# Kernel optimization log

Measured on AMD Instinct MI355X. Metric: run time of the kernel, lower is better.

The kernel has to match this reference:

```python
import jax, jax.numpy as jnp
import numpy as np

N_USERS = 100000
N_ITEMS = 50000
N_LAYERS = 3
LATENT_DIM = 64
N_INTERACTIONS = 600000
BATCH = 4096
N_TOTAL = N_USERS + N_ITEMS


def setup_inputs() -> dict:
    key = jax.random.key(0)
    k_e, k_u, k_p, k_n = jax.random.split(key, 4)

    # --- build bipartite interaction graph (numpy, host-side like scipy in the original) ---
    rng = np.random.default_rng(0)
    u = rng.integers(0, N_USERS, size=N_INTERACTIONS)
    i = rng.integers(0, N_ITEMS, size=N_INTERACTIONS) + N_USERS
    # symmetrize: A[u, i] = 1 and A[i, u] = 1
    row = np.concatenate([u, i]).astype(np.int32)
    col = np.concatenate([i, u]).astype(np.int32)
    # symmetric degree normalization: D^{-1/2} A D^{-1/2}
    deg = np.bincount(row, minlength=N_TOTAL).astype(np.float32)
    d_inv = np.power(deg + 1e-9, -0.5)
    d_inv[np.isinf(d_inv)] = 0.0
    vals = (d_inv[row] * d_inv[col]).astype(np.float32)

    # Xavier-uniform init for E0 (fan_in = fan_out = dims of the weight matrix)
    limit = float(np.sqrt(6.0 / (N_TOTAL + LATENT_DIM)))
    E0 = jax.random.uniform(k_e, (N_TOTAL, LATENT_DIM), jnp.float32, -limit, limit)

    return {
        "users": jax.random.randint(k_u, (BATCH,), 0, N_USERS),
        "pos_items": jax.random.randint(k_p, (BATCH,), 0, N_ITEMS),
        "neg_items": jax.random.randint(k_n, (BATCH,), 0, N_ITEMS),
        "E0": E0,
        "adj_row": jnp.asarray(row),
        "adj_col": jnp.asarray(col),
        "adj_vals": jnp.asarray(vals),
    }


def reference(users, pos_items, neg_items, E0, adj_row, adj_col, adj_vals):
    # SpMM via gather + segment-sum: out[r] = sum_{e: row[e]=r} vals[e] * E[col[e]]
    def spmm(E):
        return jax.ops.segment_sum(adj_vals[:, None] * E[adj_col], adj_row,
                                   num_segments=N_TOTAL)

    # layer propagation with running sum (mean over layer stack)
    E_k = E0
    acc = E0
    for _ in range(N_LAYERS):
        E_k = spmm(E_k)
        acc = acc + E_k
    final_emb = acc / (N_LAYERS + 1)  # [N_TOTAL, D]

    user_emb = final_emb[:N_USERS]
    item_emb = final_emb[N_USERS:]

    u_emb = user_emb[users]
    pos_emb = item_emb[pos_items]
    neg_emb = item_emb[neg_items]
    u_emb0 = E0[users]
    pos_emb0 = E0[N_USERS + pos_items]
    neg_emb0 = E0[N_USERS + neg_items]
    return (u_emb, pos_emb, neg_emb, u_emb0, pos_emb0, neg_emb0)
```

## Files before the change

kernel.cpp:

```cpp
#include <hip/hip_runtime.h>
#include <hip/hip_fp16.h>

#define LATENT 64
#define N_USERS_C 100000

#define BROWS 128
#define LOG_BROWS 7
#define NBUCK_MAX 1280
#define NBLKA_MAX 512
#define SORT_T 256
#define SORT_E 16
#define SORT_CHUNK (SORT_T * SORT_E)
#define BUCK_CAP 4608

typedef unsigned short ushort8_t __attribute__((ext_vector_type(8)));

__device__ __forceinline__ unsigned enc_val14(float v) {
    unsigned vb = (unsigned)__float_as_int(v) + 0x1000u;
    return (((vb >> 23) - 0x77u) << 10) | ((vb >> 13) & 0x3FFu);
}
__device__ __forceinline__ float dec_val14(unsigned m) {
    return __uint_as_float(m ? ((((m >> 10) + 0x77u) << 23) | ((m & 0x3FFu) << 13)) : 0u);
}


__global__ void sortA_conv_kernel(const int* __restrict__ row, const int* __restrict__ col,
                                  const float* __restrict__ vals,
                                  unsigned* __restrict__ aux, unsigned char* __restrict__ rowloc,
                                  int* __restrict__ cntmat, int* __restrict__ srcmat,
                                  int* __restrict__ bcnt, int nnz, int nbuck, int nblkA,
                                  const float* __restrict__ E0, __half* __restrict__ E0h,
                                  int n4) {
    __shared__ int cnt[NBUCK_MAX];
    __shared__ int off[NBUCK_MAX];
    __shared__ int part[SORT_T];
    __shared__ unsigned buf[SORT_CHUNK];
    __shared__ unsigned char rbuf[SORT_CHUNK];
    int t = threadIdx.x;

    if (blockIdx.x >= nblkA) {
        int cb = blockIdx.x - nblkA;
        int base4 = cb * (SORT_T * 4);
#pragma unroll
        for (int jj = 0; jj < 4; jj++) {
            int i = base4 + jj * SORT_T + t;
            if (i < n4) {
                float4 v = ((const float4*)E0)[i];
                __half2* o = (__half2*)E0h;
                o[2 * i]     = __floats2half2_rn(v.x, v.y);
                o[2 * i + 1] = __floats2half2_rn(v.z, v.w);
            }
        }
        return;
    }

    int blk = blockIdx.x;
    int base = blk * SORT_CHUNK;

    for (int i = t; i < nbuck; i += SORT_T) cnt[i] = 0;
    __syncthreads();

    int      eb[SORT_E];
    unsigned pl[SORT_E];
    unsigned char rl8[SORT_E];
#pragma unroll
    for (int j = 0; j < SORT_E; j++) {
        int e = base + j * SORT_T + t;
        if (e < nnz) {
            int r = row[e];
            int b = r >> LOG_BROWS;
            eb[j] = b;
            pl[j] = (unsigned)col[e] | (enc_val14(vals[e]) << 18);
            rl8[j] = (unsigned char)(r & (BROWS - 1));
            atomicAdd(&cnt[b], 1);
        } else {
            eb[j] = -1;
        }
    }
    __syncthreads();

    int chunk = (nbuck + SORT_T - 1) / SORT_T;
    int lo = t * chunk, hi = lo + chunk; if (hi > nbuck) hi = nbuck;
    int s = 0;
    for (int i = lo; i < hi; i++) s += cnt[i];
    part[t] = s;
    __syncthreads();
    for (int o = 1; o < SORT_T; o <<= 1) {
        int x = (t >= o) ? part[t - o] : 0;
        __syncthreads();
        part[t] += x;
        __syncthreads();
    }
    int run = (t == 0) ? 0 : part[t - 1];
    for (int i = lo; i < hi; i++) { off[i] = run; run += cnt[i]; }
    __syncthreads();

#pragma unroll
    for (int j = 0; j < SORT_E; j++) {
        if (eb[j] >= 0) {
            int p = atomicAdd(&off[eb[j]], 1);
            buf[p] = pl[j];
            rbuf[p] = rl8[j];
        }
    }
    __syncthreads();

    for (int b = t; b < nbuck; b += SORT_T) {
        int c = cnt[b];
        int beg = off[b] - c;
        cntmat[(size_t)blk * nbuck + b] = c;
        srcmat[(size_t)blk * nbuck + b] = beg;
        if (c) atomicAdd(&bcnt[b], c);
    }
    int nvalid = nnz - base; if (nvalid > SORT_CHUNK) nvalid = SORT_CHUNK;
    for (int i = t; i < nvalid; i += SORT_T) {
        aux[base + i] = buf[i];
        rowloc[base + i] = rbuf[i];
    }
}


__global__ void sortB_kernel(const unsigned* __restrict__ aux,
                             const unsigned char* __restrict__ rowloc,
                             const int* __restrict__ cntmat, const int* __restrict__ srcmat,
                             const int* __restrict__ bcnt,
                             unsigned* __restrict__ edges, int* __restrict__ startOut,
                             int* __restrict__ origRow, int* __restrict__ slotOfRow,
                             int nblkA, int nbuck, int ntotal, int nnz) {
    __shared__ int rs[NBLKA_MAX], roff[NBLKA_MAX + 1];
    __shared__ int part[SORT_T];
    __shared__ unsigned buf[BUCK_CAP];
    __shared__ unsigned char rbuf[BUCK_CAP];
    __shared__ int cnt128[BROWS];
    __shared__ int slotOf[BROWS];
    __shared__ int rowOf[BROWS];
    __shared__ int offS[BROWS];
    __shared__ int placeOff[BROWS];
    __shared__ int dhist[64];
    int b = blockIdx.x, t = threadIdx.x;

    int sb = 0;
    for (int i = t; i < b; i += SORT_T) sb += bcnt[i];
    part[t] = sb;
    __syncthreads();
    for (int o = 1; o < SORT_T; o <<= 1) {
        int x = (t >= o) ? part[t - o] : 0;
        __syncthreads();
        part[t] += x;
        __syncthreads();
    }
    int base = part[SORT_T - 1];
    int tot = bcnt[b];
    __syncthreads();

    int rbase = b * BROWS;
    int nr = ntotal - rbase; if (nr > BROWS) nr = BROWS;

    int chunk = (nblkA + SORT_T - 1) / SORT_T;
    int lo = t * chunk, hi = lo + chunk; if (hi > nblkA) hi = nblkA;
    int rcl[8];
    int s = 0;
    for (int i = lo; i < hi; i++) {
        int c = cntmat[(size_t)i * nbuck + b];
        rcl[i - lo] = c;
        rs[i] = srcmat[(size_t)i * nbuck + b];
        s += c;
    }
    part[t] = s;
    if (t < BROWS) cnt128[t] = 0;
    if (t < 64) dhist[t] = 0;
    __syncthreads();
    for (int o = 1; o < SORT_T; o <<= 1) {
        int x = (t >= o) ? part[t - o] : 0;
        __syncthreads();
        part[t] += x;
        __syncthreads();
    }
    int run = (t == 0) ? 0 : part[t - 1];
    for (int i = lo; i < hi; i++) { roff[i] = run; run += rcl[i - lo]; }
    if (t == SORT_T - 1) roff[nblkA] = part[SORT_T - 1];
    __syncthreads();

    for (int i = t; i < tot; i += SORT_T) {
        int lo2 = 0, hi2 = nblkA;
        while (hi2 - lo2 > 1) {
            int mid = (lo2 + hi2) >> 1;
            if (roff[mid] <= i) lo2 = mid; else hi2 = mid;
        }
        size_t src = (size_t)lo2 * SORT_CHUNK + rs[lo2] + (i - roff[lo2]);
        buf[i] = aux[src];
        unsigned char rl = rowloc[src];
        rbuf[i] = rl;
        atomicAdd(&cnt128[rl], 1);
    }
    __syncthreads();

    if (t < nr) { int d = min(cnt128[t], 63); atomicAdd(&dhist[d], 1); }
    __syncthreads();
    part[t] = (t < 64) ? dhist[t] : 0;
    __syncthreads();
    for (int o = 1; o < 64; o <<= 1) {
        int x = (t >= o) ? part[t - o] : 0;
        __syncthreads();
        part[t] += x;
        __syncthreads();
    }
    if (t < 64) dhist[t] = (t == 0) ? 0 : part[t - 1];
    __syncthreads();
    if (t < nr) {
        int d = min(cnt128[t], 63);
        int sl = atomicAdd(&dhist[d], 1);
        slotOf[t] = sl;
        rowOf[sl] = t;
    }
    __syncthreads();

    part[t] = (t < nr) ? cnt128[rowOf[t]] : 0;
    __syncthreads();
    for (int o = 1; o < SORT_T; o <<= 1) {
        int x = (t >= o) ? part[t - o] : 0;
        __syncthreads();
        part[t] += x;
        __syncthreads();
    }
    if (t < nr) offS[t] = (t == 0) ? 0 : part[t - 1];
    __syncthreads();

    if (t < nr) {
        startOut[rbase + t]   = base + offS[t];
        origRow[rbase + t]    = rbase + rowOf[t];
        slotOfRow[rbase + t]  = rbase + slotOf[t];
        placeOff[t] = offS[slotOf[t]];
    }
    if (b == nbuck - 1 && t == 0) startOut[ntotal] = nnz;
    __syncthreads();

    for (int i = t; i < tot; i += SORT_T) {
        int p = atomicAdd(&placeOff[rbuf[i]], 1);
        edges[base + p] = buf[i];
    }
}


__global__ void spmm_slot(const int* __restrict__ start, const int* __restrict__ origRow,
                          const unsigned* __restrict__ edges,
                          const __half* __restrict__ Ein, __half* __restrict__ Eout,
                          int nslots) {
    int t = blockIdx.x * blockDim.x + threadIdx.x;
    int w = t >> 6;
    int lane = t & 63;
    int g = lane >> 3, l = lane & 7;
    int s = 8 * w + g;
    if (s >= nslots) return;
    int b = start[s];
    int e = start[s + 1];
    int ro = origRow[s];
    float a0 = 0.f, a1 = 0.f, a2 = 0.f, a3 = 0.f;
    float a4 = 0.f, a5 = 0.f, a6 = 0.f, a7 = 0.f;
    for (int k = (b & ~3); k < e; k += 4) {
        uint4 ev = *(const uint4*)(edges + k);
        unsigned ed[4] = { ev.x, ev.y, ev.z, ev.w };
#pragma unroll
        for (int j = 0; j < 4; j++) {
            int kk = k + j;
            if (kk < b || kk >= e) ed[j] = 0u;
        }
        ushort8_t gv[4];
#pragma unroll
        for (int j = 0; j < 4; j++) {
            gv[j] = *(const ushort8_t*)(Ein + (size_t)(ed[j] & 0x3FFFFu) * LATENT + 8 * l);
        }
#pragma unroll
        for (int j = 0; j < 4; j++) {
            float wv = dec_val14(ed[j] >> 18);
            const __half2* h2 = (const __half2*)&gv[j];
            a0 += wv * __low2float(h2[0]);
            a1 += wv * __high2float(h2[0]);
            a2 += wv * __low2float(h2[1]);
            a3 += wv * __high2float(h2[1]);
            a4 += wv * __low2float(h2[2]);
            a5 += wv * __high2float(h2[2]);
            a6 += wv * __low2float(h2[3]);
            a7 += wv * __high2float(h2[3]);
        }
    }
    union { ushort8_t u; __half2 h[4]; } o;
    o.h[0] = __floats2half2_rn(a0, a1);
    o.h[1] = __floats2half2_rn(a2, a3);
    o.h[2] = __floats2half2_rn(a4, a5);
    o.h[3] = __floats2half2_rn(a6, a7);
    *(ushort8_t*)(Eout + (size_t)ro * LATENT + 8 * l) = o.u;
}


__global__ void fin_fused(const int* __restrict__ users, const int* __restrict__ pos,
                          const int* __restrict__ neg,
                          const int* __restrict__ start, const int* __restrict__ slotOfRow,
                          const unsigned* __restrict__ edges,
                          const float* __restrict__ E0, const __half* __restrict__ E1,
                          const __half* __restrict__ E2,
                          float* __restrict__ out, int batch) {
    int t = blockIdx.x * blockDim.x + threadIdx.x;
    int w = t >> 6;
    int lane = t & 63;
    int g = lane >> 4, l = lane & 15;
    int i = 4 * w + g;
    int nent = 3 * batch;
    if (i >= nent) return;
    int grp = i / batch;
    int bb = i - grp * batch;
    int r = (grp == 0) ? users[bb] : (grp == 1) ? (N_USERS_C + pos[bb]) : (N_USERS_C + neg[bb]);
    int s = slotOfRow[r];
    int b = start[s];
    int e = start[s + 1];
    float a0 = 0.f, a1 = 0.f, a2 = 0.f, a3 = 0.f;
    for (int k = (b & ~3); k < e; k += 4) {
        uint4 ev = *(const uint4*)(edges + k);
        unsigned ed[4] = { ev.x, ev.y, ev.z, ev.w };
#pragma unroll
        for (int j = 0; j < 4; j++) {
            int kk = k + j;
            if (kk < b || kk >= e) ed[j] = 0u;
        }
        ushort4 gv[4];
#pragma unroll
        for (int j = 0; j < 4; j++) {
            gv[j] = *(const ushort4*)(E2 + (size_t)(ed[j] & 0x3FFFFu) * LATENT + 4 * l);
        }
#pragma unroll
        for (int j = 0; j < 4; j++) {
            float wv = dec_val14(ed[j] >> 18);
            const __half2* h2 = (const __half2*)&gv[j];
            a0 += wv * __low2float(h2[0]);
            a1 += wv * __high2float(h2[0]);
            a2 += wv * __low2float(h2[1]);
            a3 += wv * __high2float(h2[1]);
        }
    }
    size_t idx = (size_t)r * LATENT + 4 * l;
    float4 e0v = *(const float4*)(E0 + idx);
    ushort4 e1u = *(const ushort4*)(E1 + idx);
    ushort4 e2u = *(const ushort4*)(E2 + idx);
    const __half2* h1 = (const __half2*)&e1u;
    const __half2* h2v = (const __half2*)&e2u;
    float4 res;
    res.x = 0.25f * (e0v.x + __low2float(h1[0])  + __low2float(h2v[0])  + a0);
    res.y = 0.25f * (e0v.y + __high2float(h1[0]) + __high2float(h2v[0]) + a1);
    res.z = 0.25f * (e0v.z + __low2float(h1[1])  + __low2float(h2v[1])  + a2);
    res.w = 0.25f * (e0v.w + __high2float(h1[1]) + __high2float(h2v[1]) + a3);
    int total = nent * LATENT;
    *(float4*)(out + (size_t)i * LATENT + 4 * l) = res;
    *(float4*)(out + total + (size_t)i * LATENT + 4 * l) = e0v;
}

extern "C" void kernel_launch(void* const* d_in, const int* in_sizes, int n_in,
                              void* d_out, int out_size, void* d_ws, size_t ws_size,
                              hipStream_t stream) {
    const int*   users = (const int*)d_in[0];
    const int*   pos   = (const int*)d_in[1];
    const int*   neg   = (const int*)d_in[2];
    const float* E0    = (const float*)d_in[3];
    const int*   row   = (const int*)d_in[4];
    const int*   col   = (const int*)d_in[5];
    const float* vals  = (const float*)d_in[6];
    float*       out   = (float*)d_out;

    const int batch  = in_sizes[0];
    const int nnz    = in_sizes[4];
    const int ntotal = in_sizes[3] / LATENT;
    const int nbuck  = (ntotal + BROWS - 1) / BROWS;
    const int nblkA  = (nnz + SORT_CHUNK - 1) / SORT_CHUNK;

    auto align256 = [](size_t x) { return (x + 255) & ~(size_t)255; };

    const size_t hbufBytes = align256((size_t)ntotal * LATENT * sizeof(__half));
    const size_t edgeBytes = align256((size_t)nnz * sizeof(unsigned) + 16);
    const size_t auxBytes  = align256((size_t)nnz * sizeof(unsigned));
    const size_t matBytes  = align256((size_t)nblkA * nbuck * sizeof(int));
    const size_t stBytes   = align256((size_t)(ntotal + 1) * sizeof(int));
    const size_t bsBytes   = align256((size_t)(nbuck + 1) * sizeof(int));

    char* p = (char*)d_ws;
    __half* E0h      = (__half*)p;          p += hbufBytes;
    __half* bufA     = (__half*)p;          p += hbufBytes;
    __half* bufB     = (__half*)p;          p += hbufBytes;
    __half* bufC     = (__half*)p;          p += hbufBytes;
    unsigned* edges  = (unsigned*)p;        p += edgeBytes;
    int*    startA   = (int*)p;             p += stBytes;
    int*    origRow  = (int*)p;             p += stBytes;
    int*    slotOfRw = (int*)p;             p += stBytes;
    int*    bcnt     = (int*)p;             p += bsBytes;
    unsigned*      aux    = (unsigned*)bufC;
    unsigned char* rowloc = (unsigned char*)((char*)bufC + auxBytes);
    int* cntmat = (int*)bufB;
    int* srcmat = (int*)((char*)bufB + matBytes);

    hipMemsetAsync(bcnt, 0, (size_t)nbuck * sizeof(int), stream);

    const int threads = 256;
    const int slotWaves = (ntotal + 7) / 8;
    const int spBlocks = (slotWaves * 64 + threads - 1) / threads;
    const int nent = 3 * batch;
    const int fBlocks = (((nent + 3) / 4) * 64 + threads - 1) / threads;
    const int n4 = ntotal * LATENT / 4;
    const int cBlocks4 = (n4 + SORT_T * 4 - 1) / (SORT_T * 4);

    sortA_conv_kernel<<<nblkA + cBlocks4, SORT_T, 0, stream>>>(
        row, col, vals, aux, rowloc, cntmat, srcmat, bcnt, nnz, nbuck, nblkA,
        E0, E0h, n4);
    sortB_kernel<<<nbuck, SORT_T, 0, stream>>>(aux, rowloc, cntmat, srcmat, bcnt,
                                               edges, startA, origRow, slotOfRw,
                                               nblkA, nbuck, ntotal, nnz);

    spmm_slot<<<spBlocks, threads, 0, stream>>>(startA, origRow, edges, E0h, bufA, ntotal);
    spmm_slot<<<spBlocks, threads, 0, stream>>>(startA, origRow, edges, bufA, bufB, ntotal);
    fin_fused<<<fBlocks, threads, 0, stream>>>(users, pos, neg, startA, slotOfRw, edges,
                                               E0, bufA, bufB, out, batch);
}
```

Measured before the change: 187.4 us.

## Fuse first SpMM layer into bucket sort kernel and vectorize edge loads

The first propagation layer now runs inside the second sort kernel: each block processes its freshly sorted bucket of 128 rows right after scattering the edges, which removes one kernel launch and one pass that re-reads the start and row-mapping arrays. The first sort kernel also loads row, column and value as int4/float4 quads instead of scalars. In exchange, the sort kernel's runtime grows with the gather work, and that work runs with only 4 waves per block and limited occupancy because of the kernel's large shared memory footprint. The edges it reads back were just written by the same block, which relies on the barrier for visibility.

```diff
diff --git a/kernel.cpp b/kernel.cpp
--- a/kernel.cpp
+++ b/kernel.cpp
@@ -63,18 +63,44 @@
     int      eb[SORT_E];
     unsigned pl[SORT_E];
     unsigned char rl8[SORT_E];
-#pragma unroll
-    for (int j = 0; j < SORT_E; j++) {
-        int e = base + j * SORT_T + t;
-        if (e < nnz) {
-            int r = row[e];
-            int b = r >> LOG_BROWS;
-            eb[j] = b;
-            pl[j] = (unsigned)col[e] | (enc_val14(vals[e]) << 18);
-            rl8[j] = (unsigned char)(r & (BROWS - 1));
-            atomicAdd(&cnt[b], 1);
+    int quadbase = base >> 2;
+#pragma unroll
+    for (int jq = 0; jq < SORT_E / 4; jq++) {
+        int q = quadbase + jq * SORT_T + t;
+        int e0 = 4 * q;
+        if (e0 + 3 < nnz) {
+            int4   r4 = ((const int4*)row)[q];
+            int4   c4 = ((const int4*)col)[q];
+            float4 v4 = ((const float4*)vals)[q];
+            int   rr[4] = { r4.x, r4.y, r4.z, r4.w };
+            int   cc[4] = { c4.x, c4.y, c4.z, c4.w };
+            float vv[4] = { v4.x, v4.y, v4.z, v4.w };
+#pragma unroll
+            for (int jj = 0; jj < 4; jj++) {
+                int j = 4 * jq + jj;
+                int r = rr[jj];
+                int b = r >> LOG_BROWS;
+                eb[j] = b;
+                pl[j] = (unsigned)cc[jj] | (enc_val14(vv[jj]) << 18);
+                rl8[j] = (unsigned char)(r & (BROWS - 1));
+                atomicAdd(&cnt[b], 1);
+            }
         } else {
-            eb[j] = -1;
+#pragma unroll
+            for (int jj = 0; jj < 4; jj++) {
+                int j = 4 * jq + jj;
+                int e = e0 + jj;
+                if (e < nnz) {
+                    int r = row[e];
+                    int b = r >> LOG_BROWS;
+                    eb[j] = b;
+                    pl[j] = (unsigned)col[e] | (enc_val14(vals[e]) << 18);
+                    rl8[j] = (unsigned char)(r & (BROWS - 1));
+                    atomicAdd(&cnt[b], 1);
+                } else {
+                    eb[j] = -1;
+                }
+            }
         }
     }
     __syncthreads();
@@ -120,13 +146,14 @@
 }
 
 
-__global__ void sortB_kernel(const unsigned* __restrict__ aux,
-                             const unsigned char* __restrict__ rowloc,
-                             const int* __restrict__ cntmat, const int* __restrict__ srcmat,
-                             const int* __restrict__ bcnt,
-                             unsigned* __restrict__ edges, int* __restrict__ startOut,
-                             int* __restrict__ origRow, int* __restrict__ slotOfRow,
-                             int nblkA, int nbuck, int ntotal, int nnz) {
+__global__ void sortB_spmm1_kernel(const unsigned* __restrict__ aux,
+                                   const unsigned char* __restrict__ rowloc,
+                                   const int* __restrict__ cntmat, const int* __restrict__ srcmat,
+                                   const int* __restrict__ bcnt,
+                                   unsigned* __restrict__ edges, int* __restrict__ startOut,
+                                   int* __restrict__ origRow, int* __restrict__ slotOfRow,
+                                   const __half* __restrict__ E0h, __half* __restrict__ E1,
+                                   int nblkA, int nbuck, int ntotal, int nnz) {
     __shared__ int rs[NBLKA_MAX], roff[NBLKA_MAX + 1];
     __shared__ int part[SORT_T];
     __shared__ unsigned buf[BUCK_CAP];
@@ -238,6 +265,53 @@
     for (int i = t; i < tot; i += SORT_T) {
         int p = atomicAdd(&placeOff[rbuf[i]], 1);
         edges[base + p] = buf[i];
+    }
+    __syncthreads();
+
+    {
+        int wv = t >> 6;
+        int lane = t & 63;
+        int g = lane >> 3, l = lane & 7;
+        for (int sl = 8 * wv + g; sl < nr; sl += 32) {
+            int bb = base + offS[sl];
+            int ee = bb + cnt128[rowOf[sl]];
+            int ro = rbase + rowOf[sl];
+            float a0 = 0.f, a1 = 0.f, a2 = 0.f, a3 = 0.f;
+            float a4 = 0.f, a5 = 0.f, a6 = 0.f, a7 = 0.f;
+            for (int k = (bb & ~3); k < ee; k += 4) {
+                uint4 ev = *(const uint4*)(edges + k);
+                unsigned ed[4] = { ev.x, ev.y, ev.z, ev.w };
+#pragma unroll
+                for (int j = 0; j < 4; j++) {
+                    int kk = k + j;
+                    if (kk < bb || kk >= ee) ed[j] = 0u;
+                }
+                ushort8_t gv[4];
+#pragma unroll
+                for (int j = 0; j < 4; j++) {
+                    gv[j] = *(const ushort8_t*)(E0h + (size_t)(ed[j] & 0x3FFFFu) * LATENT + 8 * l);
+                }
+#pragma unroll
+                for (int j = 0; j < 4; j++) {
+                    float wv2 = dec_val14(ed[j] >> 18);
+                    const __half2* h2 = (const __half2*)&gv[j];
+                    a0 += wv2 * __low2float(h2[0]);
+                    a1 += wv2 * __high2float(h2[0]);
+                    a2 += wv2 * __low2float(h2[1]);
+                    a3 += wv2 * __high2float(h2[1]);
+                    a4 += wv2 * __low2float(h2[2]);
+                    a5 += wv2 * __high2float(h2[2]);
+                    a6 += wv2 * __low2float(h2[3]);
+                    a7 += wv2 * __high2float(h2[3]);
+                }
+            }
+            union { ushort8_t u; __half2 h[4]; } o;
+            o.h[0] = __floats2half2_rn(a0, a1);
+            o.h[1] = __floats2half2_rn(a2, a3);
+            o.h[2] = __floats2half2_rn(a4, a5);
+            o.h[3] = __floats2half2_rn(a6, a7);
+            *(ushort8_t*)(E1 + (size_t)ro * LATENT + 8 * l) = o.u;
+        }
     }
 }
 
@@ -408,11 +482,11 @@
     sortA_conv_kernel<<<nblkA + cBlocks4, SORT_T, 0, stream>>>(
         row, col, vals, aux, rowloc, cntmat, srcmat, bcnt, nnz, nbuck, nblkA,
         E0, E0h, n4);
-    sortB_kernel<<<nbuck, SORT_T, 0, stream>>>(aux, rowloc, cntmat, srcmat, bcnt,
-                                               edges, startA, origRow, slotOfRw,
-                                               nblkA, nbuck, ntotal, nnz);
-
-    spmm_slot<<<spBlocks, threads, 0, stream>>>(startA, origRow, edges, E0h, bufA, ntotal);
+    sortB_spmm1_kernel<<<nbuck, SORT_T, 0, stream>>>(aux, rowloc, cntmat, srcmat, bcnt,
+                                                     edges, startA, origRow, slotOfRw,
+                                                     E0h, bufA,
+                                                     nblkA, nbuck, ntotal, nnz);
+
     spmm_slot<<<spBlocks, threads, 0, stream>>>(startA, origRow, edges, bufA, bufB, ntotal);
     fin_fused<<<fBlocks, threads, 0, stream>>>(users, pos, neg, startA, slotOfRw, edges,
                                                E0, bufA, bufB, out, batch);
```

Result: faster. 181.3 us (-3.3%).
